# Optimization experiments

Measured on AMD Instinct MI355X. Metric: run time of the kernel, lower is better.

Reference implementation:

```python
import jax, jax.numpy as jnp
import numpy as np

N_TOKENS = 32768
INPUT_DIM = 1024
HIDDEN_DIM = 256
NUM_EXPERTS = 64
TOP_K = 2


def setup_inputs() -> dict:
    key = jax.random.key(0)
    kx, k1, k2, kb1, kb2 = jax.random.split(key, 5)
    # torch nn.Linear init scale ~ U(-1/sqrt(fan_in), 1/sqrt(fan_in)); use small normals
    x = jax.random.normal(kx, (N_TOKENS, INPUT_DIM), dtype=jnp.float32)
    w1 = jax.random.normal(k1, (HIDDEN_DIM, INPUT_DIM), dtype=jnp.float32) / np.sqrt(INPUT_DIM)
    b1 = jax.random.normal(kb1, (HIDDEN_DIM,), dtype=jnp.float32) * 0.01
    w2 = jax.random.normal(k2, (NUM_EXPERTS, HIDDEN_DIM), dtype=jnp.float32) / np.sqrt(HIDDEN_DIM)
    b2 = jax.random.normal(kb2, (NUM_EXPERTS,), dtype=jnp.float32) * 0.01
    return {"x": x, "w1": w1, "b1": b1, "w2": w2, "b2": b2}


def reference(x, w1, b1, w2, b2):
    # logits = Linear -> ReLU -> Linear
    h = jax.nn.relu(jnp.einsum("nd,hd->nh", x, w1) + b1)       # [N, hidden]
    logits = jnp.einsum("nh,eh->ne", h, w2) + b2               # [N, experts]
    top_k_logits, top_k_indices = jax.lax.top_k(logits, TOP_K)  # [N, k]
    top_k_gates = jax.nn.softmax(top_k_logits, axis=-1)
    return top_k_indices, top_k_gates
```

## Files before the change

kernel.cpp:

```cpp
#include <hip/hip_runtime.h>
#include <math.h>

#define N_TOK 32768
#define IN_DIM 1024
#define HID 256
#define NE 64

union SMem {
    struct { float Xs[32][64]; float Ws[32][256]; } a;
    struct { float Hs[128][64]; float W2s[32][64]; } b;
    float Ls[64][67];
};

__global__ __launch_bounds__(256, 2)
void moe_gate_fused(const float* __restrict__ x,  const float* __restrict__ w1,
                    const float* __restrict__ b1, const float* __restrict__ w2,
                    const float* __restrict__ b2, float* __restrict__ out)
{
    __shared__ SMem sm;

    const int tid = threadIdx.x;
    const int t0  = blockIdx.x * 64;
    const int tg  = tid >> 5;
    const int hg  = tid & 31;

    float acc[8][8];
    #pragma unroll
    for (int i = 0; i < 8; ++i)
        #pragma unroll
        for (int j = 0; j < 8; ++j) acc[i][j] = 0.f;

    #pragma unroll 1
    for (int c = 0; c < 32; ++c) {
        const int k0 = c * 32;
        #pragma unroll
        for (int r = 0; r < 2; ++r) {
            int slot = tid + 256 * r;
            int t = slot >> 3, kq = (slot & 7) * 4;
            float4 v = *(const float4*)(x + (size_t)(t0 + t) * IN_DIM + k0 + kq);
            int col = (((t >> 2) ^ (kq >> 2)) << 2) | (t & 3);
            sm.a.Xs[kq + 0][col] = v.x;
            sm.a.Xs[kq + 1][col] = v.y;
            sm.a.Xs[kq + 2][col] = v.z;
            sm.a.Xs[kq + 3][col] = v.w;
        }
        #pragma unroll
        for (int r = 0; r < 8; ++r) {
            int slot = tid + 256 * r;
            int hh = slot >> 3, kq = (slot & 7) * 4;
            float4 v = *(const float4*)(w1 + (size_t)hh * IN_DIM + k0 + kq);
            int col = (((hh >> 2) ^ (kq >> 2)) << 2) | (hh & 3);
            sm.a.Ws[kq + 0][col] = v.x;
            sm.a.Ws[kq + 1][col] = v.y;
            sm.a.Ws[kq + 2][col] = v.z;
            sm.a.Ws[kq + 3][col] = v.w;
        }
        __syncthreads();

        #pragma unroll
        for (int m = 0; m < 8; ++m) {
            const float* xb0 = &sm.a.Xs[0][(((tg * 2)     ^ m) << 2)];
            const float* xb1 = &sm.a.Xs[0][(((tg * 2 + 1) ^ m) << 2)];
            const float* wb0 = &sm.a.Ws[0][(( hg ^ m)        << 2)];
            const float* wb1 = &sm.a.Ws[0][((((hg ^ m) + 32)) << 2)];
            #pragma unroll
            for (int kk = 0; kk < 4; ++kk) {
                int k = m * 4 + kk;
                float4 xv0 = *(const float4*)(xb0 + k * 64);
                float4 xv1 = *(const float4*)(xb1 + k * 64);
                float4 wv0 = *(const float4*)(wb0 + k * 256);
                float4 wv1 = *(const float4*)(wb1 + k * 256);
                float xv[8] = {xv0.x, xv0.y, xv0.z, xv0.w, xv1.x, xv1.y, xv1.z, xv1.w};
                float wv[8] = {wv0.x, wv0.y, wv0.z, wv0.w, wv1.x, wv1.y, wv1.z, wv1.w};
                #pragma unroll
                for (int i = 0; i < 8; ++i)
                    #pragma unroll
                    for (int j = 0; j < 8; ++j)
                        acc[i][j] = fmaf(xv[i], wv[j], acc[i][j]);
            }
        }
        __syncthreads();
    }

    {
        float4 bb0 = *(const float4*)(b1 + hg * 4);
        float4 bb1 = *(const float4*)(b1 + 128 + hg * 4);
        float bias1[8] = {bb0.x, bb0.y, bb0.z, bb0.w, bb1.x, bb1.y, bb1.z, bb1.w};
        #pragma unroll
        for (int i = 0; i < 8; ++i)
            #pragma unroll
            for (int j = 0; j < 8; ++j)
                acc[i][j] = fmaxf(acc[i][j] + bias1[j], 0.f);
    }

    const int ta = tid >> 4;
    const int eb = tid & 15;

    float acc2[4][4];
    #pragma unroll
    for (int i = 0; i < 4; ++i)
        #pragma unroll
        for (int j = 0; j < 4; ++j) acc2[i][j] = 0.f;

    #pragma unroll
    for (int p = 0; p < 2; ++p) {
        #pragma unroll
        for (int i = 0; i < 8; ++i) {
            int t = tg * 8 + i;
            int col = (((t >> 2) ^ (hg & 15)) << 2) | (t & 3);
            #pragma unroll
            for (int jj = 0; jj < 4; ++jj) {
                int hl = hg * 4 + jj;
                sm.b.Hs[hl][col] = acc[i][p * 4 + jj];
            }
        }
        #pragma unroll 1
        for (int c4 = 0; c4 < 4; ++c4) {
            #pragma unroll
            for (int r = 0; r < 2; ++r) {
                int slot = tid + 256 * r;
                int e = slot >> 3, kq = (slot & 7) * 4;
                float4 v = *(const float4*)(w2 + (size_t)e * HID + p * 128 + c4 * 32 + kq);
                int col = (((e >> 2) ^ (kq >> 2)) << 2) | (e & 3);
                sm.b.W2s[kq + 0][col] = v.x;
                sm.b.W2s[kq + 1][col] = v.y;
                sm.b.W2s[kq + 2][col] = v.z;
                sm.b.W2s[kq + 3][col] = v.w;
            }
            __syncthreads();
            #pragma unroll
            for (int m = 0; m < 8; ++m) {
                const float* wb = &sm.b.W2s[0][((eb ^ m) << 2)];
                #pragma unroll
                for (int kk = 0; kk < 4; ++kk) {
                    int k  = m * 4 + kk;
                    int hl = c4 * 32 + k;
                    float4 hv = *(const float4*)&sm.b.Hs[hl][((ta ^ ((hl >> 2) & 15)) << 2)];
                    float4 wv = *(const float4*)(wb + k * 64);
                    float hvv[4] = {hv.x, hv.y, hv.z, hv.w};
                    float wvv[4] = {wv.x, wv.y, wv.z, wv.w};
                    #pragma unroll
                    for (int i = 0; i < 4; ++i)
                        #pragma unroll
                        for (int j = 0; j < 4; ++j)
                            acc2[i][j] = fmaf(hvv[i], wvv[j], acc2[i][j]);
                }
            }
            __syncthreads();
        }
    }

    {
        float4 b2v = *(const float4*)(b2 + eb * 4);
        float bb2[4] = {b2v.x, b2v.y, b2v.z, b2v.w};
        #pragma unroll
        for (int i = 0; i < 4; ++i)
            #pragma unroll
            for (int j = 0; j < 4; ++j)
                sm.Ls[ta * 4 + i][eb * 4 + j] = acc2[i][j] + bb2[j];
    }
    __syncthreads();

    if (tid < 64) {
        const int t = tid;
        float m1 = -INFINITY, m2 = -INFINITY;
        int i1 = 0, i2 = 0;
        #pragma unroll 8
        for (int e = 0; e < NE; ++e) {
            float v = sm.Ls[t][e];
            if (v > m1)      { m2 = m1; i2 = i1; m1 = v; i1 = e; }
            else if (v > m2) { m2 = v; i2 = e; }
        }
        float e2  = expf(m2 - m1);
        float inv = 1.f / (1.f + e2);
        int gt = t0 + t;
        out[(size_t)gt * 2 + 0] = (float)i1;
        out[(size_t)gt * 2 + 1] = (float)i2;
        out[(size_t)2 * N_TOK + (size_t)gt * 2 + 0] = inv;
        out[(size_t)2 * N_TOK + (size_t)gt * 2 + 1] = e2 * inv;
    }
}

extern "C" void kernel_launch(void* const* d_in, const int* in_sizes, int n_in,
                              void* d_out, int out_size, void* d_ws, size_t ws_size,
                              hipStream_t stream) {
    const float* x  = (const float*)d_in[0];
    const float* w1 = (const float*)d_in[1];
    const float* b1 = (const float*)d_in[2];
    const float* w2 = (const float*)d_in[3];
    const float* b2 = (const float*)d_in[4];
    float* out = (float*)d_out;

    moe_gate_fused<<<N_TOK / 64, 256, 0, stream>>>(x, w1, b1, w2, b2, out);
}
```

Baseline: 371.8 us.

## Stream first GEMM from global memory with pre-transposed W1 instead of LDS tiles

```diff
diff --git a/kernel.cpp b/kernel.cpp
--- a/kernel.cpp
+++ b/kernel.cpp
@@ -6,120 +6,137 @@
 #define HID 256
 #define NE 64
 
+__global__ __launch_bounds__(256)
+void transpose_w1(const float* __restrict__ w1, float* __restrict__ w1t)
+{
+    __shared__ float tile[32][33];
+    const int k0 = blockIdx.x * 32;
+    const int h0 = blockIdx.y * 32;
+    const int j  = threadIdx.x & 31;
+    const int i0 = threadIdx.x >> 5;
+    #pragma unroll
+    for (int r = 0; r < 4; ++r) {
+        int i = i0 + r * 8;
+        tile[i][j] = w1[(size_t)(h0 + i) * IN_DIM + k0 + j];
+    }
+    __syncthreads();
+    #pragma unroll
+    for (int r = 0; r < 4; ++r) {
+        int i = i0 + r * 8;
+        w1t[(size_t)(k0 + i) * HID + h0 + j] = tile[j][i];
+    }
+}
+
 union SMem {
-    struct { float Xs[32][64]; float Ws[32][256]; } a;
     struct { float Hs[128][64]; float W2s[32][64]; } b;
     float Ls[64][67];
 };
 
 __global__ __launch_bounds__(256, 2)
-void moe_gate_fused(const float* __restrict__ x,  const float* __restrict__ w1,
-                    const float* __restrict__ b1, const float* __restrict__ w2,
-                    const float* __restrict__ b2, float* __restrict__ out)
+void moe_gate(const float* __restrict__ x,  const float* __restrict__ w1t,
+              const float* __restrict__ b1, const float* __restrict__ w2,
+              const float* __restrict__ b2, float* __restrict__ out)
 {
     __shared__ SMem sm;
 
     const int tid = threadIdx.x;
+    const int w   = tid >> 6;
+    const int l   = tid & 63;
     const int t0  = blockIdx.x * 64;
-    const int tg  = tid >> 5;
-    const int hg  = tid & 31;
-
-    float acc[8][8];
-    #pragma unroll
-    for (int i = 0; i < 8; ++i)
-        #pragma unroll
-        for (int j = 0; j < 8; ++j) acc[i][j] = 0.f;
+
+    const float* xb = x + (size_t)(t0 + w * 16) * IN_DIM;
+    const float* wb = w1t + l * 4;
+
+    float acc[16][4];
+    #pragma unroll
+    for (int t = 0; t < 16; ++t)
+        #pragma unroll
+        for (int j = 0; j < 4; ++j) acc[t][j] = 0.f;
+
+    float2 xA[16], xB[16];
+    float4 wA0, wA1, wB0, wB1;
+    #pragma unroll
+    for (int t = 0; t < 16; ++t) xA[t] = *(const float2*)(xb + (size_t)t * IN_DIM + 0);
+    #pragma unroll
+    for (int t = 0; t < 16; ++t) xB[t] = *(const float2*)(xb + (size_t)t * IN_DIM + 2);
+    wA0 = *(const float4*)(wb + 0 * HID);
+    wA1 = *(const float4*)(wb + 1 * HID);
+    wB0 = *(const float4*)(wb + 2 * HID);
+    wB1 = *(const float4*)(wb + 3 * HID);
+
+#define FMA_GROUP(XV, W0, W1)                                    \
+    _Pragma("unroll")                                            \
+    for (int t = 0; t < 16; ++t) {                               \
+        acc[t][0] = fmaf(XV[t].x, W0.x, acc[t][0]);              \
+        acc[t][1] = fmaf(XV[t].x, W0.y, acc[t][1]);              \
+        acc[t][2] = fmaf(XV[t].x, W0.z, acc[t][2]);              \
+        acc[t][3] = fmaf(XV[t].x, W0.w, acc[t][3]);              \
+        acc[t][0] = fmaf(XV[t].y, W1.x, acc[t][0]);              \
+        acc[t][1] = fmaf(XV[t].y, W1.y, acc[t][1]);              \
+        acc[t][2] = fmaf(XV[t].y, W1.z, acc[t][2]);              \
+        acc[t][3] = fmaf(XV[t].y, W1.w, acc[t][3]);              \
+    }
 
     #pragma unroll 1
-    for (int c = 0; c < 32; ++c) {
-        const int k0 = c * 32;
-        #pragma unroll
-        for (int r = 0; r < 2; ++r) {
-            int slot = tid + 256 * r;
-            int t = slot >> 3, kq = (slot & 7) * 4;
-            float4 v = *(const float4*)(x + (size_t)(t0 + t) * IN_DIM + k0 + kq);
-            int col = (((t >> 2) ^ (kq >> 2)) << 2) | (t & 3);
-            sm.a.Xs[kq + 0][col] = v.x;
-            sm.a.Xs[kq + 1][col] = v.y;
-            sm.a.Xs[kq + 2][col] = v.z;
-            sm.a.Xs[kq + 3][col] = v.w;
-        }
-        #pragma unroll
-        for (int r = 0; r < 8; ++r) {
-            int slot = tid + 256 * r;
-            int hh = slot >> 3, kq = (slot & 7) * 4;
-            float4 v = *(const float4*)(w1 + (size_t)hh * IN_DIM + k0 + kq);
-            int col = (((hh >> 2) ^ (kq >> 2)) << 2) | (hh & 3);
-            sm.a.Ws[kq + 0][col] = v.x;
-            sm.a.Ws[kq + 1][col] = v.y;
-            sm.a.Ws[kq + 2][col] = v.z;
-            sm.a.Ws[kq + 3][col] = v.w;
-        }
-        __syncthreads();
-
-        #pragma unroll
-        for (int m = 0; m < 8; ++m) {
-            const float* xb0 = &sm.a.Xs[0][(((tg * 2)     ^ m) << 2)];
-            const float* xb1 = &sm.a.Xs[0][(((tg * 2 + 1) ^ m) << 2)];
-            const float* wb0 = &sm.a.Ws[0][(( hg ^ m)        << 2)];
-            const float* wb1 = &sm.a.Ws[0][((((hg ^ m) + 32)) << 2)];
-            #pragma unroll
-            for (int kk = 0; kk < 4; ++kk) {
-                int k = m * 4 + kk;
-                float4 xv0 = *(const float4*)(xb0 + k * 64);
-                float4 xv1 = *(const float4*)(xb1 + k * 64);
-                float4 wv0 = *(const float4*)(wb0 + k * 256);
-                float4 wv1 = *(const float4*)(wb1 + k * 256);
-                float xv[8] = {xv0.x, xv0.y, xv0.z, xv0.w, xv1.x, xv1.y, xv1.z, xv1.w};
-                float wv[8] = {wv0.x, wv0.y, wv0.z, wv0.w, wv1.x, wv1.y, wv1.z, wv1.w};
+    for (int g = 0; g < 510; g += 2) {
+        const int k = g * 2;
+        FMA_GROUP(xA, wA0, wA1)
+        #pragma unroll
+        for (int t = 0; t < 16; ++t)
+            xA[t] = *(const float2*)(xb + (size_t)t * IN_DIM + k + 4);
+        wA0 = *(const float4*)(wb + (size_t)(k + 4) * HID);
+        wA1 = *(const float4*)(wb + (size_t)(k + 5) * HID);
+
+        FMA_GROUP(xB, wB0, wB1)
+        #pragma unroll
+        for (int t = 0; t < 16; ++t)
+            xB[t] = *(const float2*)(xb + (size_t)t * IN_DIM + k + 6);
+        wB0 = *(const float4*)(wb + (size_t)(k + 6) * HID);
+        wB1 = *(const float4*)(wb + (size_t)(k + 7) * HID);
+    }
+    FMA_GROUP(xA, wA0, wA1)
+    FMA_GROUP(xB, wB0, wB1)
+#undef FMA_GROUP
+
+    {
+        float4 bb = *(const float4*)(b1 + l * 4);
+        float bias1[4] = {bb.x, bb.y, bb.z, bb.w};
+        #pragma unroll
+        for (int t = 0; t < 16; ++t)
+            #pragma unroll
+            for (int j = 0; j < 4; ++j)
+                acc[t][j] = fmaxf(acc[t][j] + bias1[j], 0.f);
+    }
+
+    const int ta = tid >> 4;
+    const int eb = tid & 15;
+
+    float acc2[4][4];
+    #pragma unroll
+    for (int i = 0; i < 4; ++i)
+        #pragma unroll
+        for (int j = 0; j < 4; ++j) acc2[i][j] = 0.f;
+
+    #pragma unroll
+    for (int p = 0; p < 2; ++p) {
+        if ((l >> 5) == p) {
+            const int hl_base = (l & 31) * 4;
+            #pragma unroll
+            for (int t = 0; t < 16; ++t) {
+                int tt  = w * 16 + t;
+                int col = (((tt >> 2) ^ (l & 15)) << 2) | (tt & 3);
                 #pragma unroll
-                for (int i = 0; i < 8; ++i)
-                    #pragma unroll
-                    for (int j = 0; j < 8; ++j)
-                        acc[i][j] = fmaf(xv[i], wv[j], acc[i][j]);
+                for (int jj = 0; jj < 4; ++jj)
+                    sm.b.Hs[hl_base + jj][col] = acc[t][jj];
             }
         }
         __syncthreads();
-    }
-
-    {
-        float4 bb0 = *(const float4*)(b1 + hg * 4);
-        float4 bb1 = *(const float4*)(b1 + 128 + hg * 4);
-        float bias1[8] = {bb0.x, bb0.y, bb0.z, bb0.w, bb1.x, bb1.y, bb1.z, bb1.w};
-        #pragma unroll
-        for (int i = 0; i < 8; ++i)
-            #pragma unroll
-            for (int j = 0; j < 8; ++j)
-                acc[i][j] = fmaxf(acc[i][j] + bias1[j], 0.f);
-    }
-
-    const int ta = tid >> 4;
-    const int eb = tid & 15;
-
-    float acc2[4][4];
-    #pragma unroll
-    for (int i = 0; i < 4; ++i)
-        #pragma unroll
-        for (int j = 0; j < 4; ++j) acc2[i][j] = 0.f;
-
-    #pragma unroll
-    for (int p = 0; p < 2; ++p) {
-        #pragma unroll
-        for (int i = 0; i < 8; ++i) {
-            int t = tg * 8 + i;
-            int col = (((t >> 2) ^ (hg & 15)) << 2) | (t & 3);
-            #pragma unroll
-            for (int jj = 0; jj < 4; ++jj) {
-                int hl = hg * 4 + jj;
-                sm.b.Hs[hl][col] = acc[i][p * 4 + jj];
-            }
-        }
         #pragma unroll 1
         for (int c4 = 0; c4 < 4; ++c4) {
             #pragma unroll
             for (int r = 0; r < 2; ++r) {
                 int slot = tid + 256 * r;
-                int e = slot >> 3, kq = (slot & 7) * 4;
+                int e  = slot >> 3, kq = (slot & 7) * 4;
                 float4 v = *(const float4*)(w2 + (size_t)e * HID + p * 128 + c4 * 32 + kq);
                 int col = (((e >> 2) ^ (kq >> 2)) << 2) | (e & 3);
                 sm.b.W2s[kq + 0][col] = v.x;
@@ -130,13 +147,13 @@
             __syncthreads();
             #pragma unroll
             for (int m = 0; m < 8; ++m) {
-                const float* wb = &sm.b.W2s[0][((eb ^ m) << 2)];
+                const float* wbp = &sm.b.W2s[0][((eb ^ m) << 2)];
                 #pragma unroll
                 for (int kk = 0; kk < 4; ++kk) {
                     int k  = m * 4 + kk;
                     int hl = c4 * 32 + k;
                     float4 hv = *(const float4*)&sm.b.Hs[hl][((ta ^ ((hl >> 2) & 15)) << 2)];
-                    float4 wv = *(const float4*)(wb + k * 64);
+                    float4 wv = *(const float4*)(wbp + k * 64);
                     float hvv[4] = {hv.x, hv.y, hv.z, hv.w};
                     float wvv[4] = {wv.x, wv.y, wv.z, wv.w};
                     #pragma unroll
@@ -190,6 +207,8 @@
     const float* w2 = (const float*)d_in[3];
     const float* b2 = (const float*)d_in[4];
     float* out = (float*)d_out;
-
-    moe_gate_fused<<<N_TOK / 64, 256, 0, stream>>>(x, w1, b1, w2, b2, out);
+    float* w1t = (float*)d_ws;
+
+    transpose_w1<<<dim3(32, 8), 256, 0, stream>>>(w1, w1t);
+    moe_gate<<<N_TOK / 64, 256, 0, stream>>>(x, w1t, b1, w2, b2, out);
 }
```

Measured after the change: 503.6 us. 35.5% more time.

## Halve token tile per block and read second-layer weights from global memory

Applied to the files above, without the earlier changes.

```diff
diff --git a/kernel.cpp b/kernel.cpp
--- a/kernel.cpp
+++ b/kernel.cpp
@@ -7,22 +7,21 @@
 #define NE 64
 
 union SMem {
-    struct { float Xs[32][64]; float Ws[32][256]; } a;
-    struct { float Hs[128][64]; float W2s[32][64]; } b;
-    float Ls[64][67];
+    struct { float Xs[32][32]; float Ws[32][256]; } a;
+    float Hs[32][260];
 };
 
-__global__ __launch_bounds__(256, 2)
-void moe_gate_fused(const float* __restrict__ x,  const float* __restrict__ w1,
-                    const float* __restrict__ b1, const float* __restrict__ w2,
-                    const float* __restrict__ b2, float* __restrict__ out)
+__global__ __launch_bounds__(128, 2)
+void moe_gate(const float* __restrict__ x,  const float* __restrict__ w1,
+              const float* __restrict__ b1, const float* __restrict__ w2,
+              const float* __restrict__ b2, float* __restrict__ out)
 {
     __shared__ SMem sm;
 
     const int tid = threadIdx.x;
-    const int t0  = blockIdx.x * 64;
     const int tg  = tid >> 5;
     const int hg  = tid & 31;
+    const int t0  = blockIdx.x * 32;
 
     float acc[8][8];
     #pragma unroll
@@ -35,7 +34,7 @@
         const int k0 = c * 32;
         #pragma unroll
         for (int r = 0; r < 2; ++r) {
-            int slot = tid + 256 * r;
+            int slot = tid + 128 * r;
             int t = slot >> 3, kq = (slot & 7) * 4;
             float4 v = *(const float4*)(x + (size_t)(t0 + t) * IN_DIM + k0 + kq);
             int col = (((t >> 2) ^ (kq >> 2)) << 2) | (t & 3);
@@ -45,8 +44,8 @@
             sm.a.Xs[kq + 3][col] = v.w;
         }
         #pragma unroll
-        for (int r = 0; r < 8; ++r) {
-            int slot = tid + 256 * r;
+        for (int r = 0; r < 16; ++r) {
+            int slot = tid + 128 * r;
             int hh = slot >> 3, kq = (slot & 7) * 4;
             float4 v = *(const float4*)(w1 + (size_t)hh * IN_DIM + k0 + kq);
             int col = (((hh >> 2) ^ (kq >> 2)) << 2) | (hh & 3);
@@ -61,13 +60,13 @@
         for (int m = 0; m < 8; ++m) {
             const float* xb0 = &sm.a.Xs[0][(((tg * 2)     ^ m) << 2)];
             const float* xb1 = &sm.a.Xs[0][(((tg * 2 + 1) ^ m) << 2)];
-            const float* wb0 = &sm.a.Ws[0][(( hg ^ m)        << 2)];
+            const float* wb0 = &sm.a.Ws[0][(( hg ^ m)         << 2)];
             const float* wb1 = &sm.a.Ws[0][((((hg ^ m) + 32)) << 2)];
             #pragma unroll
             for (int kk = 0; kk < 4; ++kk) {
                 int k = m * 4 + kk;
-                float4 xv0 = *(const float4*)(xb0 + k * 64);
-                float4 xv1 = *(const float4*)(xb1 + k * 64);
+                float4 xv0 = *(const float4*)(xb0 + k * 32);
+                float4 xv1 = *(const float4*)(xb1 + k * 32);
                 float4 wv0 = *(const float4*)(wb0 + k * 256);
                 float4 wv1 = *(const float4*)(wb1 + k * 256);
                 float xv[8] = {xv0.x, xv0.y, xv0.z, xv0.w, xv1.x, xv1.y, xv1.z, xv1.w};
@@ -93,8 +92,21 @@
                 acc[i][j] = fmaxf(acc[i][j] + bias1[j], 0.f);
     }
 
-    const int ta = tid >> 4;
-    const int eb = tid & 15;
+    #pragma unroll
+    for (int i = 0; i < 8; ++i) {
+        *(float4*)&sm.Hs[tg * 8 + i][hg * 4] =
+            make_float4(acc[i][0], acc[i][1], acc[i][2], acc[i][3]);
+        *(float4*)&sm.Hs[tg * 8 + i][128 + hg * 4] =
+            make_float4(acc[i][4], acc[i][5], acc[i][6], acc[i][7]);
+    }
+    __syncthreads();
+
+    const int tp = tid >> 4;
+    const int e4 = tid & 15;
+
+    const float* hp[4] = { &sm.Hs[tp * 4 + 0][0], &sm.Hs[tp * 4 + 1][0],
+                           &sm.Hs[tp * 4 + 2][0], &sm.Hs[tp * 4 + 3][0] };
+    const float* w2p = w2 + (size_t)(e4 * 4) * HID;
 
     float acc2[4][4];
     #pragma unroll
@@ -102,82 +114,61 @@
         #pragma unroll
         for (int j = 0; j < 4; ++j) acc2[i][j] = 0.f;
 
-    #pragma unroll
-    for (int p = 0; p < 2; ++p) {
+    #pragma unroll 2
+    for (int k4 = 0; k4 < 64; ++k4) {
+        const int k = k4 * 4;
+        float hvv[4][4], evv[4][4];
         #pragma unroll
-        for (int i = 0; i < 8; ++i) {
-            int t = tg * 8 + i;
-            int col = (((t >> 2) ^ (hg & 15)) << 2) | (t & 3);
+        for (int i = 0; i < 4; ++i)
+            *(float4*)&hvv[i][0] = *(const float4*)(hp[i] + k);
+        #pragma unroll
+        for (int j = 0; j < 4; ++j)
+            *(float4*)&evv[j][0] = *(const float4*)(w2p + (size_t)j * HID + k);
+        #pragma unroll
+        for (int d = 0; d < 4; ++d)
             #pragma unroll
-            for (int jj = 0; jj < 4; ++jj) {
-                int hl = hg * 4 + jj;
-                sm.b.Hs[hl][col] = acc[i][p * 4 + jj];
-            }
-        }
-        #pragma unroll 1
-        for (int c4 = 0; c4 < 4; ++c4) {
-            #pragma unroll
-            for (int r = 0; r < 2; ++r) {
-                int slot = tid + 256 * r;
-                int e = slot >> 3, kq = (slot & 7) * 4;
-                float4 v = *(const float4*)(w2 + (size_t)e * HID + p * 128 + c4 * 32 + kq);
-                int col = (((e >> 2) ^ (kq >> 2)) << 2) | (e & 3);
-                sm.b.W2s[kq + 0][col] = v.x;
-                sm.b.W2s[kq + 1][col] = v.y;
-                sm.b.W2s[kq + 2][col] = v.z;
-                sm.b.W2s[kq + 3][col] = v.w;
-            }
-            __syncthreads();
-            #pragma unroll
-            for (int m = 0; m < 8; ++m) {
-                const float* wb = &sm.b.W2s[0][((eb ^ m) << 2)];
+            for (int i = 0; i < 4; ++i)
                 #pragma unroll
-                for (int kk = 0; kk < 4; ++kk) {
-                    int k  = m * 4 + kk;
-                    int hl = c4 * 32 + k;
-                    float4 hv = *(const float4*)&sm.b.Hs[hl][((ta ^ ((hl >> 2) & 15)) << 2)];
-                    float4 wv = *(const float4*)(wb + k * 64);
-                    float hvv[4] = {hv.x, hv.y, hv.z, hv.w};
-                    float wvv[4] = {wv.x, wv.y, wv.z, wv.w};
-                    #pragma unroll
-                    for (int i = 0; i < 4; ++i)
-                        #pragma unroll
-                        for (int j = 0; j < 4; ++j)
-                            acc2[i][j] = fmaf(hvv[i], wvv[j], acc2[i][j]);
-                }
-            }
-            __syncthreads();
-        }
+                for (int j = 0; j < 4; ++j)
+                    acc2[i][j] = fmaf(hvv[i][d], evv[j][d], acc2[i][j]);
     }
 
-    {
-        float4 b2v = *(const float4*)(b2 + eb * 4);
-        float bb2[4] = {b2v.x, b2v.y, b2v.z, b2v.w};
-        #pragma unroll
-        for (int i = 0; i < 4; ++i)
-            #pragma unroll
-            for (int j = 0; j < 4; ++j)
-                sm.Ls[ta * 4 + i][eb * 4 + j] = acc2[i][j] + bb2[j];
-    }
-    __syncthreads();
-
-    if (tid < 64) {
-        const int t = tid;
+    float4 b2v = *(const float4*)(b2 + e4 * 4);
+    #pragma unroll
+    for (int i = 0; i < 4; ++i) {
+        float v[4] = {acc2[i][0] + b2v.x, acc2[i][1] + b2v.y,
+                      acc2[i][2] + b2v.z, acc2[i][3] + b2v.w};
         float m1 = -INFINITY, m2 = -INFINITY;
         int i1 = 0, i2 = 0;
-        #pragma unroll 8
-        for (int e = 0; e < NE; ++e) {
-            float v = sm.Ls[t][e];
-            if (v > m1)      { m2 = m1; i2 = i1; m1 = v; i1 = e; }
-            else if (v > m2) { m2 = v; i2 = e; }
+        #pragma unroll
+        for (int j = 0; j < 4; ++j) {
+            int e = e4 * 4 + j;
+            if (v[j] > m1)      { m2 = m1; i2 = i1; m1 = v[j]; i1 = e; }
+            else if (v[j] > m2) { m2 = v[j]; i2 = e; }
         }
-        float e2  = expf(m2 - m1);
-        float inv = 1.f / (1.f + e2);
-        int gt = t0 + t;
-        out[(size_t)gt * 2 + 0] = (float)i1;
-        out[(size_t)gt * 2 + 1] = (float)i2;
-        out[(size_t)2 * N_TOK + (size_t)gt * 2 + 0] = inv;
-        out[(size_t)2 * N_TOK + (size_t)gt * 2 + 1] = e2 * inv;
+        #pragma unroll
+        for (int off = 1; off < 16; off <<= 1) {
+            float om1 = __shfl_xor(m1, off);
+            int   oi1 = __shfl_xor(i1, off);
+            float om2 = __shfl_xor(m2, off);
+            int   oi2 = __shfl_xor(i2, off);
+            bool bwin = (om1 > m1) || (om1 == m1 && oi1 < i1);
+            float c1v = bwin ? om1 : m1;  int c1i = bwin ? oi1 : i1;
+            float lv  = bwin ? m1  : om1; int li  = bwin ? i1  : oi1;
+            float w2v = bwin ? om2 : m2;  int w2i = bwin ? oi2 : i2;
+            bool s = (lv > w2v) || (lv == w2v && li < w2i);
+            m1 = c1v; i1 = c1i;
+            m2 = s ? lv : w2v; i2 = s ? li : w2i;
+        }
+        if (e4 == 0) {
+            float ex  = expf(m2 - m1);
+            float inv = 1.f / (1.f + ex);
+            int gt = t0 + tp * 4 + i;
+            out[(size_t)gt * 2 + 0] = (float)i1;
+            out[(size_t)gt * 2 + 1] = (float)i2;
+            out[(size_t)2 * N_TOK + (size_t)gt * 2 + 0] = inv;
+            out[(size_t)2 * N_TOK + (size_t)gt * 2 + 1] = ex * inv;
+        }
     }
 }
 
@@ -191,5 +182,5 @@
     const float* b2 = (const float*)d_in[4];
     float* out = (float*)d_out;
 
-    moe_gate_fused<<<N_TOK / 64, 256, 0, stream>>>(x, w1, b1, w2, b2, out);
+    moe_gate<<<N_TOK / 32, 128, 0, stream>>>(x, w1, b1, w2, b2, out);
 }
```

After: 412.4 us. +10.9%, slower.
